# Kernel optimization log

Hardware: AMD Instinct MI355X
Metric: run time of the kernel (lower is better)

## Reference

```python
import jax, jax.numpy as jnp
import numpy as np

N_ITER = 3

def setup_inputs() -> dict:
    key = jax.random.key(0)
    k1, k2 = jax.random.split(key)
    x = jax.random.normal(k1, (8, 1024, 512), dtype=jnp.float32)
    W = jax.random.normal(k2, (4, 512, 512), dtype=jnp.float32)
    return {"x": x, "W": W}

def reference(x, W):
    # x: [B, N, D], W: [H, D, D]
    B, N, D = x.shape
    H = W.shape[0]
    scale = D ** (-0.5)
    logits = jnp.zeros((B, H, N, N), dtype=x.dtype)
    rw = None
    for _ in range(N_ITER):
        rw = jax.nn.softmax(logits, axis=-1)              # [B, H, N, N]
        # per-head bilinear scores: (x @ W_h) @ x^T * scale, batched over heads
        logits = jnp.einsum('bnd,hde,bme->bhnm', x, W, x) * scale
    # routing_weights @ x, then mean over heads -> [B, N, D]
    out = jnp.einsum('bhnm,bmd->bhnd', rw, x)
    return jnp.mean(out, axis=1)
```

## Files before the change

### kernel.cpp

```cpp
#include <hip/hip_runtime.h>
#include <math.h>

#define B_ 8
#define N_ 1024
#define D_ 512
#define H_ 4
#define ND (N_ * D_)
#define DD (D_ * D_)
#define NN (N_ * N_)

typedef _Float16 f16;
typedef f16 f16x8 __attribute__((ext_vector_type(8)));
typedef float f32x4 __attribute__((ext_vector_type(4)));

typedef __attribute__((address_space(3))) void lds_void;
typedef __attribute__((address_space(1))) void g_void;

template<int NPROD, int LDA, int LDB, int LDC, int KTOT>
__device__ __forceinline__ void pair_core(
    const f16* __restrict__ A, const f16* __restrict__ B0,
    const f16* __restrict__ B1, f16* __restrict__ Ch, float scale,
    int n0, int c0)
{
    __shared__ f16 sA[256 * 32];
    __shared__ f16 sB0[128 * 32];
    __shared__ f16 sB1[(NPROD == 2) ? 128 * 32 : 64];

    const int t = threadIdx.x;
    const int w = t >> 6;
    const int l = t & 63;
    const int lrow = l >> 2;
    const int lch  = l & 3;
    const int wr = w >> 1, wc = w & 1;
    const int fr = l & 15;
    const int fq = l >> 4;

    f32x4 acc0[4][4] = {};
    f32x4 acc1[4][4] = {};

    for (int k0 = 0; k0 < KTOT; k0 += 32) {
#pragma unroll
        for (int i = 0; i < 4; ++i) {
            const int rb  = w * 4 + i;
            const int row = rb * 16 + lrow;
            const f16* ga = A + (size_t)(n0 + row) * LDA + k0 + lch * 8;
            __builtin_amdgcn_global_load_lds((g_void*)ga, (lds_void*)(sA + rb * 512), 16, 0, 0);
        }
#pragma unroll
        for (int i = 0; i < 2; ++i) {
            const int rb  = w * 2 + i;
            const int row = rb * 16 + lrow;
            const f16* gb0 = B0 + (size_t)(c0 + row) * LDB + k0 + lch * 8;
            __builtin_amdgcn_global_load_lds((g_void*)gb0, (lds_void*)(sB0 + rb * 512), 16, 0, 0);
            if constexpr (NPROD == 2) {
                const f16* gb1 = B1 + (size_t)(c0 + row) * LDB + k0 + lch * 8;
                __builtin_amdgcn_global_load_lds((g_void*)gb1, (lds_void*)(sB1 + rb * 512), 16, 0, 0);
            }
        }
        __syncthreads();

        f16x8 a0[4], a1[4], b0[4], b1[4];
#pragma unroll
        for (int i = 0; i < 4; ++i) {
            a0[i] = *(const f16x8*)(sA + (wr * 64 + i * 16 + fr) * 32 + fq * 8);
            a1[i] = *(const f16x8*)(sA + (128 * 32) + (wr * 64 + i * 16 + fr) * 32 + fq * 8);
            b0[i] = *(const f16x8*)(sB0 + (wc * 64 + i * 16 + fr) * 32 + fq * 8);
            if constexpr (NPROD == 2)
                b1[i] = *(const f16x8*)(sB1 + (wc * 64 + i * 16 + fr) * 32 + fq * 8);
        }

#pragma unroll
        for (int i = 0; i < 4; ++i)
#pragma unroll
            for (int j = 0; j < 4; ++j) {
                acc0[i][j] = __builtin_amdgcn_mfma_f32_16x16x32_f16(a0[i], b0[j], acc0[i][j], 0, 0, 0);
                acc1[i][j] = __builtin_amdgcn_mfma_f32_16x16x32_f16(a1[i], b0[j], acc1[i][j], 0, 0, 0);
                if constexpr (NPROD == 2) {
                    acc0[i][j] = __builtin_amdgcn_mfma_f32_16x16x32_f16(a0[i], b1[j], acc0[i][j], 0, 0, 0);
                    acc1[i][j] = __builtin_amdgcn_mfma_f32_16x16x32_f16(a1[i], b1[j], acc1[i][j], 0, 0, 0);
                }
            }
        __syncthreads();
    }

#pragma unroll
    for (int i = 0; i < 4; ++i)
#pragma unroll
        for (int j = 0; j < 4; ++j)
#pragma unroll
            for (int r = 0; r < 4; ++r) {
                const int row = n0 + wr * 64 + i * 16 + fq * 4 + r;
                const int col = c0 + wc * 64 + j * 16 + fr;
                Ch[(size_t)row * LDC + col] = (f16)(acc0[i][j][r] * scale);
                Ch[(size_t)(row + 128) * LDC + col] = (f16)(acc1[i][j][r] * scale);
            }
}

__global__ __launch_bounds__(256, 2) void k_g1(
    const f16* __restrict__ xfh, const f16* __restrict__ wTh,
    f16* __restrict__ Yh)
{
    const int i = blockIdx.x;
    const int b = i & 7;
    const int li = i >> 3;
    const int h = li >> 4;
    const int n0 = ((li >> 2) & 3) * 256;
    const int e0 = (li & 3) * 128;
    const int z = b * 4 + h;
    pair_core<1, D_, D_, D_, D_>(
        xfh + (size_t)b * ND,
        wTh + (size_t)h * DD, nullptr,
        Yh + (size_t)z * ND, 1.0f, n0, e0);
}

__global__ __launch_bounds__(256, 2) void k_g2(
    const f16* __restrict__ Yh, const f16* __restrict__ xfh,
    f16* __restrict__ S)
{
    const int i = blockIdx.x;
    const int b = i & 7;
    const int li = i >> 3;
    const int h = li >> 5;
    const int n0 = ((li >> 3) & 3) * 256;
    const int m0 = (li & 7) * 128;
    const int z = b * 4 + h;
    pair_core<1, D_, D_, N_, D_>(
        Yh + (size_t)z * ND,
        xfh + (size_t)b * ND, nullptr,
        S + (size_t)z * NN, 0.044194173824159216f, n0, m0);
}

__global__ __launch_bounds__(256, 2) void k_g4(
    const f16* __restrict__ P, const f16* __restrict__ xT,
    f16* __restrict__ part)
{
    const int i = blockIdx.x;
    const int b = i & 7;
    const int li = i >> 3;
    const int h = li >> 4;
    const int n0 = ((li >> 2) & 3) * 256;
    const int d0 = (li & 3) * 128;
    const int z = b * 4 + h;
    pair_core<1, N_, N_, D_, N_>(
        P + (size_t)z * NN,
        xT + (size_t)b * ND, nullptr,
        part + (size_t)z * ND, 1.0f, n0, d0);
}

__global__ __launch_bounds__(256) void k_reduce(
    const f16* __restrict__ part, float* __restrict__ out)
{
    const int i = blockIdx.x * 256 + threadIdx.x;
    const int b = i / (ND / 8);
    const int r = i - b * (ND / 8);
    const f16x8* p = (const f16x8*)part;
    f16x8 a0 = p[(size_t)(b * 4 + 0) * (ND / 8) + r];
    f16x8 a1 = p[(size_t)(b * 4 + 1) * (ND / 8) + r];
    f16x8 a2 = p[(size_t)(b * 4 + 2) * (ND / 8) + r];
    f16x8 a3 = p[(size_t)(b * 4 + 3) * (ND / 8) + r];
    float4 o0, o1;
    float* o = (float*)&o0;
#pragma unroll
    for (int k = 0; k < 4; ++k)
        o[k] = 0.25f * ((float)a0[k] + (float)a1[k] + (float)a2[k] + (float)a3[k]);
    o = (float*)&o1;
#pragma unroll
    for (int k = 0; k < 4; ++k)
        o[k] = 0.25f * ((float)a0[k+4] + (float)a1[k+4] + (float)a2[k+4] + (float)a3[k+4]);
    ((float4*)out)[(size_t)i * 2]     = o0;
    ((float4*)out)[(size_t)i * 2 + 1] = o1;
}

__global__ __launch_bounds__(256) void decomp_xw(
    const float* __restrict__ x, const float* __restrict__ W,
    f16* __restrict__ xfh, f16* __restrict__ xT, f16* __restrict__ wTh)
{
    __shared__ f16 tile[64][65];
    __shared__ float tw[64][65];
    const int t = threadIdx.x;
    const int z = blockIdx.z;
    if (z < 8) {
        const int b = z, n0 = blockIdx.y * 64, d0 = blockIdx.x * 64;
        const float* xb = x + (size_t)b * ND;
#pragma unroll
        for (int p = 0; p < 16; ++p) {
            const int idx = t + p * 256;
            const int r = idx >> 6, c = idx & 63;
            const float v = xb[(size_t)(n0 + r) * D_ + d0 + c];
            const f16 h = (f16)v;
            xfh[(size_t)b * ND + (size_t)(n0 + r) * D_ + d0 + c] = h;
            tile[r][c] = h;
        }
        __syncthreads();
#pragma unroll
        for (int p = 0; p < 16; ++p) {
            const int idx = t + p * 256;
            const int r = idx >> 6, c = idx & 63;
            xT[(size_t)b * ND + (size_t)(d0 + r) * N_ + n0 + c] = tile[c][r];
        }
    } else {
        if (blockIdx.y >= 8) return;
        const int h = z - 8, d0 = blockIdx.y * 64, e0 = blockIdx.x * 64;
        const float* Wh = W + (size_t)h * DD;
#pragma unroll
        for (int p = 0; p < 16; ++p) {
            const int idx = t + p * 256;
            const int r = idx >> 6, c = idx & 63;
            tw[r][c] = Wh[(size_t)(d0 + r) * D_ + e0 + c];
        }
        __syncthreads();
#pragma unroll
        for (int p = 0; p < 16; ++p) {
            const int idx = t + p * 256;
            const int r = idx >> 6, c = idx & 63;
            wTh[(size_t)h * DD + (size_t)(e0 + r) * D_ + d0 + c] = (f16)tw[c][r];
        }
    }
}

__global__ __launch_bounds__(256) void softmax_wave(
    const f16* __restrict__ S, f16* __restrict__ P)
{
    const int wave = threadIdx.x >> 6;
    const int l = threadIdx.x & 63;
    const int i = blockIdx.x;
    const int b = i & 7;
    const int li = i >> 3;
    const int h = li >> 8;
    const int rg = li & 255;
    const size_t row = (size_t)(b * 4 + h) * N_ + rg * 4 + wave;

    const f16x8* p = (const f16x8*)(S + row * N_);
    f16x8 v0 = p[l * 2], v1 = p[l * 2 + 1];

    float f[16];
#pragma unroll
    for (int k = 0; k < 8; ++k) { f[k] = (float)v0[k]; f[k + 8] = (float)v1[k]; }

    float m = f[0];
#pragma unroll
    for (int k = 1; k < 16; ++k) m = fmaxf(m, f[k]);
#pragma unroll
    for (int o = 32; o > 0; o >>= 1) m = fmaxf(m, __shfl_xor(m, o));

    float s = 0.f;
#pragma unroll
    for (int k = 0; k < 16; ++k) { f[k] = __expf(f[k] - m); s += f[k]; }
#pragma unroll
    for (int o = 32; o > 0; o >>= 1) s += __shfl_xor(s, o);

    const float inv = 1.0f / s;
    f16x8 o0, o1;
#pragma unroll
    for (int k = 0; k < 8; ++k) {
        o0[k] = (f16)(f[k] * inv);
        o1[k] = (f16)(f[k + 8] * inv);
    }
    f16x8* q = (f16x8*)(P + row * N_);
    q[l * 2] = o0;
    q[l * 2 + 1] = o1;
}

extern "C" void kernel_launch(void* const* d_in, const int* in_sizes, int n_in,
                              void* d_out, int out_size, void* d_ws, size_t ws_size,
                              hipStream_t stream) {
    const float* x = (const float*)d_in[0];
    const float* W = (const float*)d_in[1];
    float* out = (float*)d_out;

    char* ws = (char*)d_ws;
    const size_t MB = 1024 * 1024;
    f16*   xfh = (f16*)(ws + 0 * MB);
    f16*   xT  = (f16*)(ws + 8 * MB);
    f16*   wTh = (f16*)(ws + 16 * MB);
    f16*   Yh  = (f16*)(ws + 20 * MB);
    f16*   S   = (f16*)(ws + 52 * MB);
    f16*   P   = (f16*)(ws + 116 * MB);
    f16*   part = S;

    decomp_xw<<<dim3(8, 16, 12), 256, 0, stream>>>(x, W, xfh, xT, wTh);

    k_g1<<<dim3(512), 256, 0, stream>>>(xfh, wTh, Yh);
    k_g2<<<dim3(1024), 256, 0, stream>>>(Yh, xfh, S);
    softmax_wave<<<dim3(B_ * H_ * N_ / 4), 256, 0, stream>>>(S, P);
    k_g4<<<dim3(512), 256, 0, stream>>>(P, xT, part);
    k_reduce<<<dim3((B_ * ND / 8) / 256), 256, 0, stream>>>(part, out);
}
```

Measured before the change: 207.6 us.

## Double-buffer LDS tiles in GEMM core to overlap global loads with MFMA

Replaces the single-buffered load-sync-compute loop in the shared GEMM core with ping-pong LDS buffers, issuing the next K-slice's global_load_lds while the current slice runs its MFMAs. One barrier per 32-wide K-step remains, but load latency can now hide behind compute. The unused two-product B1 path is removed. LDS use doubles to about 48KB per block, which may limit occupancy at the requested two blocks per CU.

```diff
diff --git a/kernel.cpp b/kernel.cpp
--- a/kernel.cpp
+++ b/kernel.cpp
@@ -16,15 +16,54 @@
 typedef __attribute__((address_space(3))) void lds_void;
 typedef __attribute__((address_space(1))) void g_void;
 
-template<int NPROD, int LDA, int LDB, int LDC, int KTOT>
+
+#define STAGE_P(SA_, SB_, K0_)                                              \
+    {                                                                        \
+        _Pragma("unroll")                                                    \
+        for (int i_ = 0; i_ < 4; ++i_) {                                     \
+            const int rb_  = w * 4 + i_;                                     \
+            const int row_ = rb_ * 16 + lrow;                                \
+            const f16* ga_ = A + (size_t)(n0 + row_) * LDA + (K0_) + lch * 8;\
+            __builtin_amdgcn_global_load_lds((g_void*)ga_,                   \
+                (lds_void*)(SA_ + rb_ * 512), 16, 0, 0);                     \
+        }                                                                    \
+        _Pragma("unroll")                                                    \
+        for (int i_ = 0; i_ < 2; ++i_) {                                     \
+            const int rb_  = w * 2 + i_;                                     \
+            const int row_ = rb_ * 16 + lrow;                                \
+            const f16* gb_ = B0 + (size_t)(c0 + row_) * LDB + (K0_) + lch * 8;\
+            __builtin_amdgcn_global_load_lds((g_void*)gb_,                   \
+                (lds_void*)(SB_ + rb_ * 512), 16, 0, 0);                     \
+        }                                                                    \
+    }
+
+#define COMPUTE_P(SA_, SB_)                                                  \
+    {                                                                        \
+        f16x8 a0_[4], a1_[4], b0_[4];                                        \
+        _Pragma("unroll")                                                    \
+        for (int i_ = 0; i_ < 4; ++i_) {                                     \
+            a0_[i_] = *(const f16x8*)(SA_ + (wr * 64 + i_ * 16 + fr) * 32 + fq * 8); \
+            a1_[i_] = *(const f16x8*)(SA_ + (128 * 32) + (wr * 64 + i_ * 16 + fr) * 32 + fq * 8); \
+            b0_[i_] = *(const f16x8*)(SB_ + (wc * 64 + i_ * 16 + fr) * 32 + fq * 8); \
+        }                                                                    \
+        _Pragma("unroll")                                                    \
+        for (int i_ = 0; i_ < 4; ++i_)                                       \
+            _Pragma("unroll")                                                \
+            for (int j_ = 0; j_ < 4; ++j_) {                                 \
+                acc0[i_][j_] = __builtin_amdgcn_mfma_f32_16x16x32_f16(a0_[i_], b0_[j_], acc0[i_][j_], 0, 0, 0); \
+                acc1[i_][j_] = __builtin_amdgcn_mfma_f32_16x16x32_f16(a1_[i_], b0_[j_], acc1[i_][j_], 0, 0, 0); \
+            }                                                                \
+    }
+
+template<int LDA, int LDB, int LDC, int KTOT>
 __device__ __forceinline__ void pair_core(
     const f16* __restrict__ A, const f16* __restrict__ B0,
-    const f16* __restrict__ B1, f16* __restrict__ Ch, float scale,
-    int n0, int c0)
-{
-    __shared__ f16 sA[256 * 32];
-    __shared__ f16 sB0[128 * 32];
-    __shared__ f16 sB1[(NPROD == 2) ? 128 * 32 : 64];
+    f16* __restrict__ Ch, float scale, int n0, int c0)
+{
+    __shared__ f16 sAa[256 * 32];
+    __shared__ f16 sAb[256 * 32];
+    __shared__ f16 sBa[128 * 32];
+    __shared__ f16 sBb[128 * 32];
 
     const int t = threadIdx.x;
     const int w = t >> 6;
@@ -38,48 +77,17 @@
     f32x4 acc0[4][4] = {};
     f32x4 acc1[4][4] = {};
 
-    for (int k0 = 0; k0 < KTOT; k0 += 32) {
-#pragma unroll
-        for (int i = 0; i < 4; ++i) {
-            const int rb  = w * 4 + i;
-            const int row = rb * 16 + lrow;
-            const f16* ga = A + (size_t)(n0 + row) * LDA + k0 + lch * 8;
-            __builtin_amdgcn_global_load_lds((g_void*)ga, (lds_void*)(sA + rb * 512), 16, 0, 0);
-        }
-#pragma unroll
-        for (int i = 0; i < 2; ++i) {
-            const int rb  = w * 2 + i;
-            const int row = rb * 16 + lrow;
-            const f16* gb0 = B0 + (size_t)(c0 + row) * LDB + k0 + lch * 8;
-            __builtin_amdgcn_global_load_lds((g_void*)gb0, (lds_void*)(sB0 + rb * 512), 16, 0, 0);
-            if constexpr (NPROD == 2) {
-                const f16* gb1 = B1 + (size_t)(c0 + row) * LDB + k0 + lch * 8;
-                __builtin_amdgcn_global_load_lds((g_void*)gb1, (lds_void*)(sB1 + rb * 512), 16, 0, 0);
-            }
-        }
-        __syncthreads();
-
-        f16x8 a0[4], a1[4], b0[4], b1[4];
-#pragma unroll
-        for (int i = 0; i < 4; ++i) {
-            a0[i] = *(const f16x8*)(sA + (wr * 64 + i * 16 + fr) * 32 + fq * 8);
-            a1[i] = *(const f16x8*)(sA + (128 * 32) + (wr * 64 + i * 16 + fr) * 32 + fq * 8);
-            b0[i] = *(const f16x8*)(sB0 + (wc * 64 + i * 16 + fr) * 32 + fq * 8);
-            if constexpr (NPROD == 2)
-                b1[i] = *(const f16x8*)(sB1 + (wc * 64 + i * 16 + fr) * 32 + fq * 8);
-        }
-
-#pragma unroll
-        for (int i = 0; i < 4; ++i)
-#pragma unroll
-            for (int j = 0; j < 4; ++j) {
-                acc0[i][j] = __builtin_amdgcn_mfma_f32_16x16x32_f16(a0[i], b0[j], acc0[i][j], 0, 0, 0);
-                acc1[i][j] = __builtin_amdgcn_mfma_f32_16x16x32_f16(a1[i], b0[j], acc1[i][j], 0, 0, 0);
-                if constexpr (NPROD == 2) {
-                    acc0[i][j] = __builtin_amdgcn_mfma_f32_16x16x32_f16(a0[i], b1[j], acc0[i][j], 0, 0, 0);
-                    acc1[i][j] = __builtin_amdgcn_mfma_f32_16x16x32_f16(a1[i], b1[j], acc1[i][j], 0, 0, 0);
-                }
-            }
+    STAGE_P(sAa, sBa, 0);
+    __syncthreads();
+
+#pragma unroll
+    for (int it = 0; it < KTOT / 64; ++it) {
+        const int k0 = it * 64;
+        STAGE_P(sAb, sBb, k0 + 32);
+        COMPUTE_P(sAa, sBa);
+        __syncthreads();
+        if (k0 + 64 < KTOT) STAGE_P(sAa, sBa, k0 + 64);
+        COMPUTE_P(sAb, sBb);
         __syncthreads();
     }
 
@@ -107,9 +115,9 @@
     const int n0 = ((li >> 2) & 3) * 256;
     const int e0 = (li & 3) * 128;
     const int z = b * 4 + h;
-    pair_core<1, D_, D_, D_, D_>(
+    pair_core<D_, D_, D_, D_>(
         xfh + (size_t)b * ND,
-        wTh + (size_t)h * DD, nullptr,
+        wTh + (size_t)h * DD,
         Yh + (size_t)z * ND, 1.0f, n0, e0);
 }
 
@@ -124,9 +132,9 @@
     const int n0 = ((li >> 3) & 3) * 256;
     const int m0 = (li & 7) * 128;
     const int z = b * 4 + h;
-    pair_core<1, D_, D_, N_, D_>(
+    pair_core<D_, D_, N_, D_>(
         Yh + (size_t)z * ND,
-        xfh + (size_t)b * ND, nullptr,
+        xfh + (size_t)b * ND,
         S + (size_t)z * NN, 0.044194173824159216f, n0, m0);
 }
 
@@ -141,9 +149,9 @@
     const int n0 = ((li >> 2) & 3) * 256;
     const int d0 = (li & 3) * 128;
     const int z = b * 4 + h;
-    pair_core<1, N_, N_, D_, N_>(
+    pair_core<N_, N_, D_, N_>(
         P + (size_t)z * NN,
-        xT + (size_t)b * ND, nullptr,
+        xT + (size_t)b * ND,
         part + (size_t)z * ND, 1.0f, n0, d0);
 }
 
```

New measurement: 207.1 us. Within noise of the previous version (-0.2%).

## Replace GEMM core with 256x256 double-buffered, swizzled, phased MFMA pipeline

Applied to the files above, without the earlier changes.

Replaces the 256x128 single-buffered GEMM core with a 256x256 tile, 512-thread kernel using K=64 steps, double-buffered LDS with async global-to-LDS loads interleaved across four compute phases, and an XOR swizzle on the LDS layout to avoid bank conflicts. It is meant to hide global load latency behind MFMA work and increase operand reuse per tile. The cost is 128KB of LDS and large accumulator register pressure, so occupancy drops and the grids shrink to 256/512 blocks.

```diff
diff --git a/kernel.cpp b/kernel.cpp
--- a/kernel.cpp
+++ b/kernel.cpp
@@ -16,135 +16,163 @@
 typedef __attribute__((address_space(3))) void lds_void;
 typedef __attribute__((address_space(1))) void g_void;
 
-template<int NPROD, int LDA, int LDB, int LDC, int KTOT>
-__device__ __forceinline__ void pair_core(
-    const f16* __restrict__ A, const f16* __restrict__ B0,
-    const f16* __restrict__ B1, f16* __restrict__ Ch, float scale,
-    int n0, int c0)
-{
-    __shared__ f16 sA[256 * 32];
-    __shared__ f16 sB0[128 * 32];
-    __shared__ f16 sB1[(NPROD == 2) ? 128 * 32 : 64];
+
+#define PHASE_(PA, PB, QR, QC, STAGE, TAIL)                                   \
+    {                                                                         \
+        f16x8 av[4][2], bv[2][2];                                             \
+        _Pragma("unroll")                                                     \
+        for (int i_ = 0; i_ < 4; ++i_) {                                      \
+            const int ra_ = (QR) * 128 + wr * 64 + i_ * 16 + fr;              \
+            av[i_][0] = *(const f16x8*)(PA + ra_ * 64 + sw0 * 8);             \
+            av[i_][1] = *(const f16x8*)(PA + ra_ * 64 + sw1 * 8);             \
+        }                                                                     \
+        _Pragma("unroll")                                                     \
+        for (int j_ = 0; j_ < 2; ++j_) {                                      \
+            const int rb_ = (QC) * 128 + wc * 32 + j_ * 16 + fr;              \
+            bv[j_][0] = *(const f16x8*)(PB + rb_ * 64 + sw0 * 8);             \
+            bv[j_][1] = *(const f16x8*)(PB + rb_ * 64 + sw1 * 8);             \
+        }                                                                     \
+        __builtin_amdgcn_sched_barrier(0);                                    \
+        STAGE;                                                                \
+        __builtin_amdgcn_s_barrier();                                         \
+        asm volatile("s_waitcnt lgkmcnt(0)" ::: "memory");                    \
+        __builtin_amdgcn_sched_barrier(0);                                    \
+        __builtin_amdgcn_s_setprio(1);                                        \
+        _Pragma("unroll")                                                     \
+        for (int i_ = 0; i_ < 4; ++i_)                                        \
+            _Pragma("unroll")                                                 \
+            for (int j_ = 0; j_ < 2; ++j_) {                                  \
+                acc[(QR)*4+i_][(QC)*2+j_] = __builtin_amdgcn_mfma_f32_16x16x32_f16(av[i_][0], bv[j_][0], acc[(QR)*4+i_][(QC)*2+j_], 0, 0, 0); \
+                acc[(QR)*4+i_][(QC)*2+j_] = __builtin_amdgcn_mfma_f32_16x16x32_f16(av[i_][1], bv[j_][1], acc[(QR)*4+i_][(QC)*2+j_], 0, 0, 0); \
+            }                                                                 \
+        __builtin_amdgcn_s_setprio(0);                                        \
+        TAIL;                                                                 \
+        __builtin_amdgcn_s_barrier();                                         \
+    }
+
+template<int LDA, int LDB, int LDC, int KTOT>
+__device__ __forceinline__ void gemm256(
+    const f16* __restrict__ A, const f16* __restrict__ B,
+    f16* __restrict__ C, float scale, int m0, int n0)
+{
+    constexpr int NT = KTOT / 64;
+    __shared__ f16 sA0[256 * 64];
+    __shared__ f16 sB0[256 * 64];
+    __shared__ f16 sA1[256 * 64];
+    __shared__ f16 sB1[256 * 64];
 
     const int t = threadIdx.x;
-    const int w = t >> 6;
-    const int l = t & 63;
-    const int lrow = l >> 2;
-    const int lch  = l & 3;
-    const int wr = w >> 1, wc = w & 1;
-    const int fr = l & 15;
-    const int fq = l >> 4;
-
-    f32x4 acc0[4][4] = {};
-    f32x4 acc1[4][4] = {};
-
-    for (int k0 = 0; k0 < KTOT; k0 += 32) {
-#pragma unroll
-        for (int i = 0; i < 4; ++i) {
-            const int rb  = w * 4 + i;
-            const int row = rb * 16 + lrow;
-            const f16* ga = A + (size_t)(n0 + row) * LDA + k0 + lch * 8;
-            __builtin_amdgcn_global_load_lds((g_void*)ga, (lds_void*)(sA + rb * 512), 16, 0, 0);
-        }
+    const int w = t >> 6, l = t & 63;
+    const int fr = l & 15, fq = l >> 4;
+    const int wr = w >> 2, wc = w & 3;
+    const int lr = l >> 3, lc = l & 7;
+    const int swc = lc ^ lr;
+    const int sw0 = fq ^ (fr & 7);
+    const int sw1 = (4 + fq) ^ (fr & 7);
+
+    f32x4 acc[8][4] = {};
+
+    auto stageA = [&](f16* buf, int half, int kt) {
 #pragma unroll
         for (int i = 0; i < 2; ++i) {
-            const int rb  = w * 2 + i;
-            const int row = rb * 16 + lrow;
-            const f16* gb0 = B0 + (size_t)(c0 + row) * LDB + k0 + lch * 8;
-            __builtin_amdgcn_global_load_lds((g_void*)gb0, (lds_void*)(sB0 + rb * 512), 16, 0, 0);
-            if constexpr (NPROD == 2) {
-                const f16* gb1 = B1 + (size_t)(c0 + row) * LDB + k0 + lch * 8;
-                __builtin_amdgcn_global_load_lds((g_void*)gb1, (lds_void*)(sB1 + rb * 512), 16, 0, 0);
+            const int r0 = half * 128 + i * 64 + w * 8;
+            const f16* g = A + (size_t)(m0 + r0 + lr) * LDA + kt * 64 + swc * 8;
+            __builtin_amdgcn_global_load_lds((g_void*)g, (lds_void*)(buf + r0 * 64), 16, 0, 0);
+        }
+    };
+    auto stageB = [&](f16* buf, int half, int kt) {
+#pragma unroll
+        for (int i = 0; i < 2; ++i) {
+            const int r0 = half * 128 + i * 64 + w * 8;
+            const f16* g = B + (size_t)(n0 + r0 + lr) * LDB + kt * 64 + swc * 8;
+            __builtin_amdgcn_global_load_lds((g_void*)g, (lds_void*)(buf + r0 * 64), 16, 0, 0);
+        }
+    };
+
+    stageA(sA0, 0, 0); stageB(sB0, 0, 0);
+    stageA(sA0, 1, 0); stageB(sB0, 1, 0);
+    if (NT > 1) { stageA(sA1, 0, 1); stageB(sB1, 0, 1); }
+    asm volatile("s_waitcnt vmcnt(4)" ::: "memory");
+    __builtin_amdgcn_s_barrier();
+
+#pragma unroll 2
+    for (int kt = 0; kt < NT; ++kt) {
+        f16* cA = (kt & 1) ? sA1 : sA0;
+        f16* cB = (kt & 1) ? sB1 : sB0;
+        f16* nA = (kt & 1) ? sA0 : sA1;
+        f16* nB = (kt & 1) ? sB0 : sB1;
+        PHASE_(cA, cB, 0, 0, { if (kt + 1 < NT) stageA(nA, 1, kt + 1); }, {});
+        PHASE_(cA, cB, 0, 1, { if (kt + 1 < NT) stageB(nB, 1, kt + 1); }, {});
+        PHASE_(cA, cB, 1, 0, { if (kt + 2 < NT) stageA(cA, 0, kt + 2); }, {});
+        PHASE_(cA, cB, 1, 1, { if (kt + 2 < NT) stageB(cB, 0, kt + 2); },
+               { if (kt + 2 < NT) { asm volatile("s_waitcnt vmcnt(4)" ::: "memory"); }
+                 else             { asm volatile("s_waitcnt vmcnt(0)" ::: "memory"); } });
+    }
+
+#pragma unroll
+    for (int ri = 0; ri < 8; ++ri)
+#pragma unroll
+        for (int cj = 0; cj < 4; ++cj)
+#pragma unroll
+            for (int rr = 0; rr < 4; ++rr) {
+                const int row = m0 + (ri >> 2) * 128 + wr * 64 + (ri & 3) * 16 + fq * 4 + rr;
+                const int col = n0 + (cj >> 1) * 128 + wc * 32 + (cj & 1) * 16 + fr;
+                C[(size_t)row * LDC + col] = (f16)(acc[ri][cj][rr] * scale);
             }
-        }
-        __syncthreads();
-
-        f16x8 a0[4], a1[4], b0[4], b1[4];
-#pragma unroll
-        for (int i = 0; i < 4; ++i) {
-            a0[i] = *(const f16x8*)(sA + (wr * 64 + i * 16 + fr) * 32 + fq * 8);
-            a1[i] = *(const f16x8*)(sA + (128 * 32) + (wr * 64 + i * 16 + fr) * 32 + fq * 8);
-            b0[i] = *(const f16x8*)(sB0 + (wc * 64 + i * 16 + fr) * 32 + fq * 8);
-            if constexpr (NPROD == 2)
-                b1[i] = *(const f16x8*)(sB1 + (wc * 64 + i * 16 + fr) * 32 + fq * 8);
-        }
-
-#pragma unroll
-        for (int i = 0; i < 4; ++i)
-#pragma unroll
-            for (int j = 0; j < 4; ++j) {
-                acc0[i][j] = __builtin_amdgcn_mfma_f32_16x16x32_f16(a0[i], b0[j], acc0[i][j], 0, 0, 0);
-                acc1[i][j] = __builtin_amdgcn_mfma_f32_16x16x32_f16(a1[i], b0[j], acc1[i][j], 0, 0, 0);
-                if constexpr (NPROD == 2) {
-                    acc0[i][j] = __builtin_amdgcn_mfma_f32_16x16x32_f16(a0[i], b1[j], acc0[i][j], 0, 0, 0);
-                    acc1[i][j] = __builtin_amdgcn_mfma_f32_16x16x32_f16(a1[i], b1[j], acc1[i][j], 0, 0, 0);
-                }
-            }
-        __syncthreads();
-    }
-
-#pragma unroll
-    for (int i = 0; i < 4; ++i)
-#pragma unroll
-        for (int j = 0; j < 4; ++j)
-#pragma unroll
-            for (int r = 0; r < 4; ++r) {
-                const int row = n0 + wr * 64 + i * 16 + fq * 4 + r;
-                const int col = c0 + wc * 64 + j * 16 + fr;
-                Ch[(size_t)row * LDC + col] = (f16)(acc0[i][j][r] * scale);
-                Ch[(size_t)(row + 128) * LDC + col] = (f16)(acc1[i][j][r] * scale);
-            }
-}
-
-__global__ __launch_bounds__(256, 2) void k_g1(
+}
+
+__global__ __launch_bounds__(512, 2) void k_g1(
     const f16* __restrict__ xfh, const f16* __restrict__ wTh,
     f16* __restrict__ Yh)
+{
+    const int i = blockIdx.x;
+    const int b = i & 7;
+    const int li = i >> 3;
+    const int h = li >> 3;
+    const int tile = li & 7;
+    const int m0 = (tile >> 1) * 256;
+    const int n0 = (tile & 1) * 256;
+    const int z = b * 4 + h;
+    gemm256<D_, D_, D_, D_>(
+        xfh + (size_t)b * ND,
+        wTh + (size_t)h * DD,
+        Yh + (size_t)z * ND, 1.0f, m0, n0);
+}
+
+__global__ __launch_bounds__(512, 2) void k_g2(
+    const f16* __restrict__ Yh, const f16* __restrict__ xfh,
+    f16* __restrict__ S)
 {
     const int i = blockIdx.x;
     const int b = i & 7;
     const int li = i >> 3;
     const int h = li >> 4;
-    const int n0 = ((li >> 2) & 3) * 256;
-    const int e0 = (li & 3) * 128;
+    const int tile = li & 15;
+    const int m0 = (tile >> 2) * 256;
+    const int n0 = (tile & 3) * 256;
     const int z = b * 4 + h;
-    pair_core<1, D_, D_, D_, D_>(
+    gemm256<D_, D_, N_, D_>(
+        Yh + (size_t)z * ND,
         xfh + (size_t)b * ND,
-        wTh + (size_t)h * DD, nullptr,
-        Yh + (size_t)z * ND, 1.0f, n0, e0);
-}
-
-__global__ __launch_bounds__(256, 2) void k_g2(
-    const f16* __restrict__ Yh, const f16* __restrict__ xfh,
-    f16* __restrict__ S)
+        S + (size_t)z * NN, 0.044194173824159216f, m0, n0);
+}
+
+__global__ __launch_bounds__(512, 2) void k_g4(
+    const f16* __restrict__ P, const f16* __restrict__ xT,
+    f16* __restrict__ part)
 {
     const int i = blockIdx.x;
     const int b = i & 7;
     const int li = i >> 3;
-    const int h = li >> 5;
-    const int n0 = ((li >> 3) & 3) * 256;
-    const int m0 = (li & 7) * 128;
+    const int h = li >> 3;
+    const int tile = li & 7;
+    const int m0 = (tile >> 1) * 256;
+    const int n0 = (tile & 1) * 256;
     const int z = b * 4 + h;
-    pair_core<1, D_, D_, N_, D_>(
-        Yh + (size_t)z * ND,
-        xfh + (size_t)b * ND, nullptr,
-        S + (size_t)z * NN, 0.044194173824159216f, n0, m0);
-}
-
-__global__ __launch_bounds__(256, 2) void k_g4(
-    const f16* __restrict__ P, const f16* __restrict__ xT,
-    f16* __restrict__ part)
-{
-    const int i = blockIdx.x;
-    const int b = i & 7;
-    const int li = i >> 3;
-    const int h = li >> 4;
-    const int n0 = ((li >> 2) & 3) * 256;
-    const int d0 = (li & 3) * 128;
-    const int z = b * 4 + h;
-    pair_core<1, N_, N_, D_, N_>(
+    gemm256<N_, N_, D_, N_>(
         P + (size_t)z * NN,
-        xT + (size_t)b * ND, nullptr,
-        part + (size_t)z * ND, 1.0f, n0, d0);
+        xT + (size_t)b * ND,
+        part + (size_t)z * ND, 1.0f, m0, n0);
 }
 
 __global__ __launch_bounds__(256) void k_reduce(
@@ -280,9 +308,9 @@
 
     decomp_xw<<<dim3(8, 16, 12), 256, 0, stream>>>(x, W, xfh, xT, wTh);
 
-    k_g1<<<dim3(512), 256, 0, stream>>>(xfh, wTh, Yh);
-    k_g2<<<dim3(1024), 256, 0, stream>>>(Yh, xfh, S);
+    k_g1<<<dim3(256), 512, 0, stream>>>(xfh, wTh, Yh);
+    k_g2<<<dim3(512), 512, 0, stream>>>(Yh, xfh, S);
     softmax_wave<<<dim3(B_ * H_ * N_ / 4), 256, 0, stream>>>(S, P);
-    k_g4<<<dim3(512), 256, 0, stream>>>(P, xT, part);
+    k_g4<<<dim3(256), 512, 0, stream>>>(P, xT, part);
     k_reduce<<<dim3((B_ * ND / 8) / 256), 256, 0, stream>>>(part, out);
 }
```

Result: no change. 208.6 us (+0.5%).
